# Kernel optimization log

Measured on AMD Instinct MI355X. Metric: run time of the kernel, lower is better.

## Reference

```python
import jax, jax.numpy as jnp
import numpy as np

TOP_K = 2
NUM_EXPERTS = 8


def setup_inputs() -> dict:
    key = jax.random.key(0)
    ks = jax.random.split(key, 9)
    B, S, N, H = 1, 8, 1024, 512
    E, I_moe, I_sh = NUM_EXPERTS, 2048 // TOP_K, 2048
    s = 0.02
    return {
        "hidden_states": jax.random.normal(ks[0], (B, S, N, H), dtype=jnp.float32),
        "gate_w": jax.random.normal(ks[1], (E, H), dtype=jnp.float32) * s,
        "expert_w1": jax.random.normal(ks[2], (E, I_moe, H), dtype=jnp.float32) * s,
        "expert_w2": jax.random.normal(ks[3], (E, H, I_moe), dtype=jnp.float32) * s,
        "expert_w3": jax.random.normal(ks[4], (E, I_moe, H), dtype=jnp.float32) * s,
        "shared_w1": jax.random.normal(ks[5], (I_sh, H), dtype=jnp.float32) * s,
        "shared_w2": jax.random.normal(ks[6], (H, I_sh), dtype=jnp.float32) * s,
        "shared_w3": jax.random.normal(ks[7], (I_sh, H), dtype=jnp.float32) * s,
        "shared_gate_w": jax.random.normal(ks[8], (1, H), dtype=jnp.float32) * s,
    }


def reference(hidden_states, gate_w, expert_w1, expert_w2, expert_w3,
              shared_w1, shared_w2, shared_w3, shared_gate_w):
    B, S, N, H = hidden_states.shape
    x = hidden_states.reshape(-1, H)                       # [T, H], T = B*S*N

    # Router: softmax in fp32, then top-k (norm_topk_prob=False).
    router_logits = x @ gate_w.T                           # [T, E]
    probs = jax.nn.softmax(router_logits.astype(jnp.float32), axis=-1)
    top_w, top_i = jax.lax.top_k(probs, TOP_K)             # [T, k]
    # Combine weight per (token, expert): zero for unselected experts.
    combine = jnp.sum(top_w[..., None] * jax.nn.one_hot(top_i, NUM_EXPERTS, dtype=probs.dtype), axis=1)
    combine = combine.astype(x.dtype)                      # [T, E]

    # Routed experts (SwiGLU FFN per expert), evaluated densely and masked
    # by the sparse combine weights (same math as gather/scatter dispatch).
    h1 = jnp.einsum('th,eih->tei', x, expert_w1)           # [T, E, I_moe]
    h3 = jnp.einsum('th,eih->tei', x, expert_w3)
    h = jax.nn.silu(h1) * h3
    expert_out = jnp.einsum('tei,ehi->teh', h, expert_w2)  # [T, E, H]
    moe_out = jnp.einsum('te,teh->th', combine, expert_out)

    # Shared expert with sigmoid gate.
    sh = (jax.nn.silu(x @ shared_w1.T) * (x @ shared_w3.T)) @ shared_w2.T
    sgate = jax.nn.sigmoid(x @ shared_gate_w.T)            # [T, 1]
    out = moe_out + sgate * sh

    return out.reshape(B, S, N, H), router_logits
```

## Files before the change

### kernel.cpp

```cpp
#include <hip/hip_runtime.h>
#include <hip/hip_bf16.h>
#include <stdint.h>
#include <math.h>

typedef __bf16 bf16;
typedef bf16 bf16x8 __attribute__((ext_vector_type(8)));
typedef bf16 bf16x4 __attribute__((ext_vector_type(4)));
typedef float f32x4 __attribute__((ext_vector_type(4)));
typedef unsigned int u32;

#define TOKENS 8192
#define HD 512
#define NE 8
#define IM 1024
#define ISH 2048
#define CAP 2560

__device__ __forceinline__ void gld16(const void* g, void* l) {
  __builtin_amdgcn_global_load_lds(
      (const __attribute__((address_space(1))) u32*)g,
      (__attribute__((address_space(3))) u32*)l, 16, 0, 0);
}

#define RT_BLOCKS (TOKENS / 4)
#define CVT_BLOCKS 3840
#define CVT_STRIDE (CVT_BLOCKS * 256)
#define F4_E  (NE * IM * HD / 4)
#define F4_S  (ISH * HD / 4)
#define F4_C1 (F4_E)
#define F4_C2 (F4_C1 + F4_E)
#define F4_C3 (F4_C2 + F4_S)
#define F4_C4 (F4_C3 + F4_S)
#define F4_C5 (F4_C4 + F4_E)
#define F4_TOT (F4_C5 + F4_S)

__launch_bounds__(256)
__global__ void router_cvt_k(const float* __restrict__ x, const float* __restrict__ gw,
                             const float* __restrict__ sgw, float* __restrict__ logits,
                             float* __restrict__ sgate, int* __restrict__ topi,
                             float* __restrict__ topw, int* __restrict__ counts,
                             bf16* __restrict__ xb,
                             const float* __restrict__ e1, const float* __restrict__ e3,
                             const float* __restrict__ s1, const float* __restrict__ s3,
                             const float* __restrict__ e2, const float* __restrict__ s2,
                             bf16* __restrict__ wdst) {
  if (blockIdx.x >= RT_BLOCKS) {
    int idx = (blockIdx.x - RT_BLOCKS) * 256 + threadIdx.x;
#pragma unroll
    for (int it = 0; it < 4; it++, idx += CVT_STRIDE) {
      const float* s; int off;
      if (idx < F4_C1)      { s = e1; off = idx; }
      else if (idx < F4_C2) { s = e3; off = idx - F4_C1; }
      else if (idx < F4_C3) { s = s1; off = idx - F4_C2; }
      else if (idx < F4_C4) { s = s3; off = idx - F4_C3; }
      else if (idx < F4_C5) { s = e2; off = idx - F4_C4; }
      else                  { s = s2; off = idx - F4_C5; }
      const float4 v = ((const float4*)s)[off];
      bf16x4 o;
      o.x = (bf16)v.x; o.y = (bf16)v.y; o.z = (bf16)v.z; o.w = (bf16)v.w;
      ((bf16x4*)wdst)[idx] = o;
    }
    return;
  }
  if (blockIdx.x == 0 && threadIdx.x < NE) counts[threadIdx.x] = 0;
  __shared__ float gws[9][512];
  for (int i = threadIdx.x; i < 9 * 512; i += 256) {
    int r = i >> 9, c = i & 511;
    float v = (r < 8) ? gw[i] : sgw[c];
    gws[r][((c & 7) << 6) | (c >> 3)] = v;
  }
  __syncthreads();
  int wave = threadIdx.x >> 6, lane = threadIdx.x & 63;
  int t = blockIdx.x * 4 + wave;
  const float* xp = x + (size_t)t * HD + lane * 8;
  float4 va = *(const float4*)xp;
  float4 vb = *(const float4*)(xp + 4);
  float xv[8] = {va.x, va.y, va.z, va.w, vb.x, vb.y, vb.z, vb.w};
  {
    bf16x8 xo;
#pragma unroll
    for (int j = 0; j < 8; j++) xo[j] = (bf16)xv[j];
    *(bf16x8*)(xb + (size_t)t * HD + lane * 8) = xo;
  }
  float acc[9];
#pragma unroll
  for (int e = 0; e < 9; e++) {
    float a = 0.f;
#pragma unroll
    for (int j = 0; j < 8; j++) a = fmaf(xv[j], gws[e][j * 64 + lane], a);
    acc[e] = a;
  }
#pragma unroll
  for (int off = 32; off > 0; off >>= 1) {
#pragma unroll
    for (int e = 0; e < 9; e++) acc[e] += __shfl_down(acc[e], off);
  }
  if (lane == 0) {
    float mx = acc[0];
#pragma unroll
    for (int e = 1; e < 8; e++) mx = fmaxf(mx, acc[e]);
    float p[8], sum = 0.f;
#pragma unroll
    for (int e = 0; e < 8; e++) { p[e] = expf(acc[e] - mx); sum += p[e]; }
    float inv = 1.f / sum;
    int i0 = 0; float b0 = p[0];
#pragma unroll
    for (int e = 1; e < 8; e++) if (p[e] > b0) { b0 = p[e]; i0 = e; }
    int i1 = -1; float b1 = -1.f;
#pragma unroll
    for (int e = 0; e < 8; e++) if (e != i0 && p[e] > b1) { b1 = p[e]; i1 = e; }
#pragma unroll
    for (int e = 0; e < 8; e++) logits[(size_t)t * 8 + e] = acc[e];
    topi[2 * t] = i0; topi[2 * t + 1] = i1;
    topw[2 * t] = b0 * inv; topw[2 * t + 1] = b1 * inv;
    sgate[t] = 1.f / (1.f + expf(-acc[8]));
  }
}

__launch_bounds__(256)
__global__ void dispatch_k(const int* __restrict__ topi, const float* __restrict__ topw,
                           int* __restrict__ counts, int* __restrict__ tok,
                           float* __restrict__ wl, int* __restrict__ pos) {
  __shared__ int lcnt[NE];
  __shared__ int lbase[NE];
  int tid = threadIdx.x;
  if (tid < NE) lcnt[tid] = 0;
  __syncthreads();
  int t = blockIdx.x * 256 + tid;
  int e0 = topi[2 * t], e1 = topi[2 * t + 1];
  float w0 = topw[2 * t], w1 = topw[2 * t + 1];
  int r0 = atomicAdd(&lcnt[e0], 1);
  int r1 = atomicAdd(&lcnt[e1], 1);
  __syncthreads();
  if (tid < NE) lbase[tid] = atomicAdd(&counts[tid], lcnt[tid]);
  __syncthreads();
  int p0 = lbase[e0] + r0;
  int p1 = lbase[e1] + r1;
  if (p0 < CAP) { tok[e0 * CAP + p0] = t; wl[e0 * CAP + p0] = w0; }
  if (p1 < CAP) { tok[e1 * CAP + p1] = t; wl[e1 * CAP + p1] = w1; }
  pos[2 * t]     = (p0 < CAP) ? e0 * CAP + p0 : -1;
  pos[2 * t + 1] = (p1 < CAP) ? e1 * CAP + p1 : -1;
}

__launch_bounds__(256, 4)
__global__ void gemm1_k(const bf16* __restrict__ X, const int* __restrict__ tokl,
                        const int* __restrict__ counts,
                        const bf16* __restrict__ e1w, const bf16* __restrict__ e3w,
                        const bf16* __restrict__ s1w, const bf16* __restrict__ s3w,
                        bf16* __restrict__ hmoe, bf16* __restrict__ hsh) {
  const bf16 *W1, *W3;
  bf16* Hout;
  const int* tl = nullptr;
  int cnt = 0, m0, n0, N;
  bool gather;
  int y = blockIdx.y;
  if (y < 160) {
    int e = y / 20, mt = y % 20;
    cnt = min(counts[e], CAP);
    if (mt * 128 >= cnt) return;
    gather = true;
    tl = tokl + e * CAP;
    W1 = e1w + (size_t)e * IM * HD;
    W3 = e3w + (size_t)e * IM * HD;
    Hout = hmoe + (size_t)e * CAP * IM;
    N = IM; m0 = mt * 128; n0 = blockIdx.x * 64;
  } else {
    int s = y - 160;
    gather = false;
    W1 = s1w; W3 = s3w; Hout = hsh; N = ISH;
    m0 = (s >> 1) * 128;
    n0 = ((s & 1) * 16 + blockIdx.x) * 64;
  }

  __shared__ __align__(16) bf16 As[2][128 * 32];
  __shared__ __align__(16) bf16 B1s[2][64 * 32];
  __shared__ __align__(16) bf16 B3s[2][64 * 32];

  int tid = threadIdx.x;
  int sr = tid >> 2;
  int colb = (tid & 3) * 16;
  int ar0, ar1;
  if (gather) {
    ar0 = tl[min(m0 + sr, cnt - 1)];
    ar1 = tl[min(m0 + 64 + sr, cnt - 1)];
  } else { ar0 = m0 + sr; ar1 = m0 + 64 + sr; }
  const char* apa = (const char*)(X + (size_t)ar0 * HD) + colb;
  const char* apb = (const char*)(X + (size_t)ar1 * HD) + colb;
  const char* bp1 = (const char*)(W1 + (size_t)(n0 + sr) * HD) + colb;
  const char* bp3 = (const char*)(W3 + (size_t)(n0 + sr) * HD) + colb;
  char* lA0a = (char*)&As[0][0] + tid * 16;
  char* lA0b = (char*)&As[1][0] + tid * 16;
  char* lA1a = (char*)&As[0][0] + 4096 + tid * 16;
  char* lA1b = (char*)&As[1][0] + 4096 + tid * 16;
  char* lB1a = (char*)&B1s[0][0] + tid * 16;
  char* lB1b = (char*)&B1s[1][0] + tid * 16;
  char* lB3a = (char*)&B3s[0][0] + tid * 16;
  char* lB3b = (char*)&B3s[1][0] + tid * 16;

  int wid = tid >> 6, lane = tid & 63;
  int wm = (wid >> 1) * 64, wn = (wid & 1) * 32;
  int lrow = lane & 15, lq = lane >> 4;

  f32x4 acc1[4][2] = {};
  f32x4 acc3[4][2] = {};

  for (int kb = 0; kb < 1024; kb += 128) {
    __syncthreads();
    gld16(apa + kb, lA0a);      gld16(apa + kb + 64, lA0b);
    gld16(apb + kb, lA1a);      gld16(apb + kb + 64, lA1b);
    gld16(bp1 + kb, lB1a);      gld16(bp1 + kb + 64, lB1b);
    gld16(bp3 + kb, lB3a);      gld16(bp3 + kb + 64, lB3b);
    __syncthreads();
#pragma unroll
    for (int ks = 0; ks < 2; ks++) {
      bf16x8 a[4], b1[2], b3[2];
#pragma unroll
      for (int i = 0; i < 4; i++)
        a[i] = *(const bf16x8*)&As[ks][(wm + i * 16 + lrow) * 32 + lq * 8];
#pragma unroll
      for (int j = 0; j < 2; j++) {
        b1[j] = *(const bf16x8*)&B1s[ks][(wn + j * 16 + lrow) * 32 + lq * 8];
        b3[j] = *(const bf16x8*)&B3s[ks][(wn + j * 16 + lrow) * 32 + lq * 8];
      }
#pragma unroll
      for (int i = 0; i < 4; i++)
#pragma unroll
        for (int j = 0; j < 2; j++) {
          acc1[i][j] = __builtin_amdgcn_mfma_f32_16x16x32_bf16(a[i], b1[j], acc1[i][j], 0, 0, 0);
          acc3[i][j] = __builtin_amdgcn_mfma_f32_16x16x32_bf16(a[i], b3[j], acc3[i][j], 0, 0, 0);
        }
    }
  }

#pragma unroll
  for (int i = 0; i < 4; i++)
#pragma unroll
    for (int r = 0; r < 4; r++) {
      int row = m0 + wm + i * 16 + lq * 4 + r;
#pragma unroll
      for (int j = 0; j < 2; j++) {
        float v1 = acc1[i][j][r], v3 = acc3[i][j][r];
        float hv = v1 / (1.f + __expf(-v1)) * v3;
        Hout[(size_t)row * N + (n0 + wn + j * 16 + lrow)] = (bf16)hv;
      }
    }
}

__launch_bounds__(256, 4)
__global__ void gemm2_k(const bf16* __restrict__ hmoe, const bf16* __restrict__ hsh,
                        const bf16* __restrict__ e2w, const bf16* __restrict__ s2w,
                        const float* __restrict__ wll, const int* __restrict__ counts,
                        bf16* __restrict__ yslot, bf16* __restrict__ ysh) {
  const bf16 *Hin, *W2;
  const float* wlp = nullptr;
  bf16* Yout;
  int cnt = 0, m0, K;
  bool weighted;
  int y = blockIdx.y;
  if (y < 64) {
    weighted = false;
    Hin = hsh; W2 = s2w; Yout = ysh; K = ISH; m0 = y * 128;
  } else {
    int e = (y - 64) / 20, mt = (y - 64) % 20;
    cnt = min(counts[e], CAP);
    if (mt * 128 >= cnt) return;
    weighted = true;
    Hin = hmoe + (size_t)e * CAP * IM;
    W2 = e2w + (size_t)e * HD * IM;
    wlp = wll + e * CAP;
    Yout = yslot + (size_t)e * CAP * HD;
    K = IM; m0 = mt * 128;
  }
  int n0 = blockIdx.x * 128;

  __shared__ __align__(16) bf16 As[2][128 * 32];
  __shared__ __align__(16) bf16 Bs[2][128 * 32];

  int tid = threadIdx.x;
  int sr = tid >> 2;
  int colb = (tid & 3) * 16;
  const char* apa = (const char*)(Hin + (size_t)(m0 + sr) * K) + colb;
  const char* apb = (const char*)(Hin + (size_t)(m0 + 64 + sr) * K) + colb;
  const char* bpa = (const char*)(W2 + (size_t)(n0 + sr) * K) + colb;
  const char* bpb = (const char*)(W2 + (size_t)(n0 + 64 + sr) * K) + colb;
  char* lA0a = (char*)&As[0][0] + tid * 16;
  char* lA0b = (char*)&As[1][0] + tid * 16;
  char* lA1a = (char*)&As[0][0] + 4096 + tid * 16;
  char* lA1b = (char*)&As[1][0] + 4096 + tid * 16;
  char* lB0a = (char*)&Bs[0][0] + tid * 16;
  char* lB0b = (char*)&Bs[1][0] + tid * 16;
  char* lB1a = (char*)&Bs[0][0] + 4096 + tid * 16;
  char* lB1b = (char*)&Bs[1][0] + 4096 + tid * 16;

  int wid = tid >> 6, lane = tid & 63;
  int wm = (wid >> 1) * 64, wn = (wid & 1) * 64;
  int lrow = lane & 15, lq = lane >> 4;

  f32x4 acc[4][4] = {};

  for (int kb = 0; kb < K * 2; kb += 128) {
    __syncthreads();
    gld16(apa + kb, lA0a);      gld16(apa + kb + 64, lA0b);
    gld16(apb + kb, lA1a);      gld16(apb + kb + 64, lA1b);
    gld16(bpa + kb, lB0a);      gld16(bpa + kb + 64, lB0b);
    gld16(bpb + kb, lB1a);      gld16(bpb + kb + 64, lB1b);
    __syncthreads();
#pragma unroll
    for (int ks = 0; ks < 2; ks++) {
      bf16x8 a[4], b[4];
#pragma unroll
      for (int i = 0; i < 4; i++) {
        a[i] = *(const bf16x8*)&As[ks][(wm + i * 16 + lrow) * 32 + lq * 8];
        b[i] = *(const bf16x8*)&Bs[ks][(wn + i * 16 + lrow) * 32 + lq * 8];
      }
#pragma unroll
      for (int i = 0; i < 4; i++)
#pragma unroll
        for (int j = 0; j < 4; j++)
          acc[i][j] = __builtin_amdgcn_mfma_f32_16x16x32_bf16(a[i], b[j], acc[i][j], 0, 0, 0);
    }
  }

#pragma unroll
  for (int i = 0; i < 4; i++)
#pragma unroll
    for (int r = 0; r < 4; r++) {
      int row = m0 + wm + i * 16 + lq * 4 + r;
      float w = weighted ? ((row < cnt) ? wlp[row] : 0.f) : 1.f;
      bf16* op = Yout + (size_t)row * HD;
#pragma unroll
      for (int j = 0; j < 4; j++)
        op[n0 + wn + j * 16 + lrow] = (bf16)(w * acc[i][j][r]);
    }
}

__launch_bounds__(256)
__global__ void combine_k(const bf16* __restrict__ yslot, const bf16* __restrict__ ysh,
                          const int* __restrict__ pos, const float* __restrict__ sgate,
                          float* __restrict__ out) {
  int wave = threadIdx.x >> 6, lane = threadIdx.x & 63;
  int t = blockIdx.x * 4 + wave;
  int p0 = pos[2 * t], p1 = pos[2 * t + 1];
  float g = sgate[t];
  int col = lane * 8;
  float acc[8];
  {
    const bf16x8 s = *(const bf16x8*)(ysh + (size_t)t * HD + col);
#pragma unroll
    for (int i = 0; i < 8; i++) acc[i] = g * (float)s[i];
  }
  if (p0 >= 0) {
    const bf16x8 v = *(const bf16x8*)(yslot + (size_t)p0 * HD + col);
#pragma unroll
    for (int i = 0; i < 8; i++) acc[i] += (float)v[i];
  }
  if (p1 >= 0) {
    const bf16x8 v = *(const bf16x8*)(yslot + (size_t)p1 * HD + col);
#pragma unroll
    for (int i = 0; i < 8; i++) acc[i] += (float)v[i];
  }
  float* op = out + (size_t)t * HD + col;
#pragma unroll
  for (int i = 0; i < 8; i++) op[i] = acc[i];
}

extern "C" void kernel_launch(void* const* d_in, const int* in_sizes, int n_in,
                              void* d_out, int out_size, void* d_ws, size_t ws_size,
                              hipStream_t stream) {
  const float* x   = (const float*)d_in[0];
  const float* gw  = (const float*)d_in[1];
  const float* ew1 = (const float*)d_in[2];
  const float* ew2 = (const float*)d_in[3];
  const float* ew3 = (const float*)d_in[4];
  const float* sw1 = (const float*)d_in[5];
  const float* sw2 = (const float*)d_in[6];
  const float* sw3 = (const float*)d_in[7];
  const float* sgw = (const float*)d_in[8];
  float* out = (float*)d_out;
  float* logits = out + (size_t)TOKENS * HD;

  char* w = (char*)d_ws;
  bf16* xb  = (bf16*)w; w += (size_t)TOKENS * HD * 2;
  bf16* e1b = (bf16*)w; w += (size_t)NE * IM * HD * 2;
  bf16* e3b = (bf16*)w; w += (size_t)NE * IM * HD * 2;
  bf16* s1b = (bf16*)w; w += (size_t)ISH * HD * 2;
  bf16* s3b = (bf16*)w; w += (size_t)ISH * HD * 2;
  bf16* e2b = (bf16*)w; w += (size_t)NE * HD * IM * 2;
  bf16* s2b = (bf16*)w; w += (size_t)HD * ISH * 2;
  float* sgate = (float*)w; w += TOKENS * 4;
  int*   topi  = (int*)w;   w += TOKENS * 2 * 4;
  float* topw  = (float*)w; w += TOKENS * 2 * 4;
  int*   counts = (int*)w;  w += 256;
  int*   tok   = (int*)w;   w += NE * CAP * 4;
  float* wl    = (float*)w; w += NE * CAP * 4;
  int*   pos   = (int*)w;   w += TOKENS * 2 * 4;
  bf16* hmoe = (bf16*)w; w += (size_t)NE * CAP * IM * 2;
  bf16* hsh  = (bf16*)w; w += (size_t)TOKENS * ISH * 2;
  bf16* yslot = xb;
  bf16* ysh   = (bf16*)((char*)xb + (size_t)NE * CAP * HD * 2);

  hipLaunchKernelGGL(router_cvt_k, dim3(RT_BLOCKS + CVT_BLOCKS), dim3(256), 0, stream,
                     x, gw, sgw, logits, sgate, topi, topw, counts, xb,
                     ew1, ew3, sw1, sw3, ew2, sw2, e1b);
  hipLaunchKernelGGL(dispatch_k, dim3(TOKENS / 256), dim3(256), 0, stream,
                     topi, topw, counts, tok, wl, pos);
  hipLaunchKernelGGL(gemm1_k, dim3(16, 160 + 128), dim3(256), 0, stream,
                     xb, tok, counts, e1b, e3b, s1b, s3b, hmoe, hsh);
  hipLaunchKernelGGL(gemm2_k, dim3(4, 64 + 160), dim3(256), 0, stream,
                     hmoe, hsh, e2b, s2b, wl, counts, yslot, ysh);
  hipLaunchKernelGGL(combine_k, dim3(TOKENS / 4), dim3(256), 0, stream,
                     yslot, ysh, pos, sgate, out);
}
```

Measured before the change: 264.0 us.

## Rewrite gate/up GEMM with 256x128 tiles, swizzled LDS and phased pipelining

```diff
diff --git a/kernel.cpp b/kernel.cpp
--- a/kernel.cpp
+++ b/kernel.cpp
@@ -142,7 +142,10 @@
   pos[2 * t + 1] = (p1 < CAP) ? e1 * CAP + p1 : -1;
 }
 
-__launch_bounds__(256, 4)
+#define LDSA(D) ((D) * 65536)
+#define LDSB(D) ((D) * 65536 + 32768)
+
+__launch_bounds__(512, 2)
 __global__ void gemm1_k(const bf16* __restrict__ X, const int* __restrict__ tokl,
                         const int* __restrict__ counts,
                         const bf16* __restrict__ e1w, const bf16* __restrict__ e3w,
@@ -154,96 +157,146 @@
   int cnt = 0, m0, n0, N;
   bool gather;
   int y = blockIdx.y;
-  if (y < 160) {
-    int e = y / 20, mt = y % 20;
+  if (y < 80) {
+    int e = y / 10, mt = y % 10;
     cnt = min(counts[e], CAP);
-    if (mt * 128 >= cnt) return;
+    if (mt * 256 >= cnt) return;
     gather = true;
     tl = tokl + e * CAP;
     W1 = e1w + (size_t)e * IM * HD;
     W3 = e3w + (size_t)e * IM * HD;
     Hout = hmoe + (size_t)e * CAP * IM;
-    N = IM; m0 = mt * 128; n0 = blockIdx.x * 64;
+    N = IM; m0 = mt * 256; n0 = blockIdx.x * 128;
   } else {
-    int s = y - 160;
+    int s = y - 80;
     gather = false;
     W1 = s1w; W3 = s3w; Hout = hsh; N = ISH;
-    m0 = (s >> 1) * 128;
-    n0 = ((s & 1) * 16 + blockIdx.x) * 64;
-  }
-
-  __shared__ __align__(16) bf16 As[2][128 * 32];
-  __shared__ __align__(16) bf16 B1s[2][64 * 32];
-  __shared__ __align__(16) bf16 B3s[2][64 * 32];
+    m0 = (s >> 1) * 256;
+    n0 = ((s & 1) * 8 + blockIdx.x) * 128;
+  }
+
+  __shared__ __align__(16) char smem[131072];
+  char* lds = (char*)smem;
 
   int tid = threadIdx.x;
-  int sr = tid >> 2;
-  int colb = (tid & 3) * 16;
-  int ar0, ar1;
+  int lane = tid & 63, wid = tid >> 6;
+  int wr = wid >> 2, wc = wid & 3;
+  int lrow = lane & 15, lq = lane >> 4;
+  int rs = (lq * 16) ^ ((lane & 4) << 3);
+  int aoff = wr * 16384 + lrow * 128 + rs;
+  int boff = 32768 + wc * 4096 + lrow * 128 + rs;
+  int rg = tid >> 3;
+  int colb = ((tid & 7) << 4) ^ (tid & 32);
+
+  const char *gA0, *gA1, *gA2, *gA3;
   if (gather) {
-    ar0 = tl[min(m0 + sr, cnt - 1)];
-    ar1 = tl[min(m0 + 64 + sr, cnt - 1)];
-  } else { ar0 = m0 + sr; ar1 = m0 + 64 + sr; }
-  const char* apa = (const char*)(X + (size_t)ar0 * HD) + colb;
-  const char* apb = (const char*)(X + (size_t)ar1 * HD) + colb;
-  const char* bp1 = (const char*)(W1 + (size_t)(n0 + sr) * HD) + colb;
-  const char* bp3 = (const char*)(W3 + (size_t)(n0 + sr) * HD) + colb;
-  char* lA0a = (char*)&As[0][0] + tid * 16;
-  char* lA0b = (char*)&As[1][0] + tid * 16;
-  char* lA1a = (char*)&As[0][0] + 4096 + tid * 16;
-  char* lA1b = (char*)&As[1][0] + 4096 + tid * 16;
-  char* lB1a = (char*)&B1s[0][0] + tid * 16;
-  char* lB1b = (char*)&B1s[1][0] + tid * 16;
-  char* lB3a = (char*)&B3s[0][0] + tid * 16;
-  char* lB3b = (char*)&B3s[1][0] + tid * 16;
-
-  int wid = tid >> 6, lane = tid & 63;
-  int wm = (wid >> 1) * 64, wn = (wid & 1) * 32;
-  int lrow = lane & 15, lq = lane >> 4;
-
-  f32x4 acc1[4][2] = {};
-  f32x4 acc3[4][2] = {};
-
-  for (int kb = 0; kb < 1024; kb += 128) {
-    __syncthreads();
-    gld16(apa + kb, lA0a);      gld16(apa + kb + 64, lA0b);
-    gld16(apb + kb, lA1a);      gld16(apb + kb + 64, lA1b);
-    gld16(bp1 + kb, lB1a);      gld16(bp1 + kb + 64, lB1b);
-    gld16(bp3 + kb, lB3a);      gld16(bp3 + kb + 64, lB3b);
-    __syncthreads();
-#pragma unroll
-    for (int ks = 0; ks < 2; ks++) {
-      bf16x8 a[4], b1[2], b3[2];
-#pragma unroll
-      for (int i = 0; i < 4; i++)
-        a[i] = *(const bf16x8*)&As[ks][(wm + i * 16 + lrow) * 32 + lq * 8];
-#pragma unroll
-      for (int j = 0; j < 2; j++) {
-        b1[j] = *(const bf16x8*)&B1s[ks][(wn + j * 16 + lrow) * 32 + lq * 8];
-        b3[j] = *(const bf16x8*)&B3s[ks][(wn + j * 16 + lrow) * 32 + lq * 8];
-      }
-#pragma unroll
-      for (int i = 0; i < 4; i++)
-#pragma unroll
-        for (int j = 0; j < 2; j++) {
-          acc1[i][j] = __builtin_amdgcn_mfma_f32_16x16x32_bf16(a[i], b1[j], acc1[i][j], 0, 0, 0);
-          acc3[i][j] = __builtin_amdgcn_mfma_f32_16x16x32_bf16(a[i], b3[j], acc3[i][j], 0, 0, 0);
-        }
-    }
-  }
-
-#pragma unroll
-  for (int i = 0; i < 4; i++)
+    gA0 = (const char*)(X + (size_t)tl[min(m0 + rg,       cnt - 1)] * HD) + colb;
+    gA1 = (const char*)(X + (size_t)tl[min(m0 + 64 + rg,  cnt - 1)] * HD) + colb;
+    gA2 = (const char*)(X + (size_t)tl[min(m0 + 128 + rg, cnt - 1)] * HD) + colb;
+    gA3 = (const char*)(X + (size_t)tl[min(m0 + 192 + rg, cnt - 1)] * HD) + colb;
+  } else {
+    gA0 = (const char*)(X + (size_t)(m0 + rg) * HD) + colb;
+    gA1 = (const char*)(X + (size_t)(m0 + 64 + rg) * HD) + colb;
+    gA2 = (const char*)(X + (size_t)(m0 + 128 + rg) * HD) + colb;
+    gA3 = (const char*)(X + (size_t)(m0 + 192 + rg) * HD) + colb;
+  }
+  const char* gBa = (const char*)(W1 + (size_t)(n0 + rg) * HD) + colb;
+  const char* gBb = (const char*)(W1 + (size_t)(n0 + 64 + rg) * HD) + colb;
+  const char* gBc = (const char*)(W3 + (size_t)(n0 + rg) * HD) + colb;
+  const char* gBd = (const char*)(W3 + (size_t)(n0 + 64 + rg) * HD) + colb;
+
+#define STG2(P0, O0, P1, O1, KT) { \
+    gld16(P0 + (KT) * 128, lds + (O0) + tid * 16); \
+    gld16(P1 + (KT) * 128, lds + (O1) + tid * 16); }
+#define STG_AQ0(D, KT) STG2(gA0, LDSA(D),         gA2, LDSA(D) + 16384, KT)
+#define STG_AQ1(D, KT) STG2(gA1, LDSA(D) + 8192,  gA3, LDSA(D) + 24576, KT)
+#define STG_B0(D, KT)  STG2(gBa, LDSB(D),         gBb, LDSB(D) + 8192,  KT)
+#define STG_B1(D, KT)  STG2(gBc, LDSB(D) + 16384, gBd, LDSB(D) + 24576, KT)
+
+  bf16x8 a[4][2], b1[2][2], b3[2][2];
+  f32x4 acc1[8][2] = {};
+  f32x4 acc3[8][2] = {};
+
+#define LD_A(D, IB) \
+  _Pragma("unroll") for (int i2 = 0; i2 < 4; i2++) \
+  _Pragma("unroll") for (int ks = 0; ks < 2; ks++) \
+    a[i2][ks] = *(const bf16x8*)(lds + (D) * 65536 + aoff + ((IB) + i2) * 2048 + ks * 64);
+#define LD_B(D, REG, EX) \
+  _Pragma("unroll") for (int j = 0; j < 2; j++) \
+  _Pragma("unroll") for (int ks = 0; ks < 2; ks++) \
+    REG[j][ks] = *(const bf16x8*)(lds + (D) * 65536 + boff + (EX) + j * 2048 + ks * 64);
+#define PH_MFMA(ACC, ILO, B) \
+  __builtin_amdgcn_s_barrier(); \
+  __builtin_amdgcn_s_setprio(1); \
+  _Pragma("unroll") for (int i2 = 0; i2 < 4; i2++) \
+  _Pragma("unroll") for (int j = 0; j < 2; j++) \
+  _Pragma("unroll") for (int ks = 0; ks < 2; ks++) \
+    ACC[(ILO) + i2][j] = __builtin_amdgcn_mfma_f32_16x16x32_bf16( \
+        a[i2][ks], B[j][ks], ACC[(ILO) + i2][j], 0, 0, 0); \
+  __builtin_amdgcn_s_setprio(0); \
+  __builtin_amdgcn_s_barrier();
+
+  STG_AQ0(0, 0); STG_B0(0, 0); STG_B1(0, 0); STG_AQ1(0, 0);
+  STG_AQ0(1, 1); STG_B1(1, 1); STG_AQ1(1, 1);
+  asm volatile("s_waitcnt vmcnt(6)" ::: "memory");
+  __builtin_amdgcn_s_barrier();
+
+#pragma unroll 1
+  for (int it = 0; it < 4; ++it) {
+    const int t2 = 2 * it + 2, t3 = 2 * it + 3;
+    const bool more = it < 3;
+    LD_A(0, 0); LD_B(0, b1, 0);
+    STG_B0(1, 2 * it + 1);
+    PH_MFMA(acc1, 0, b1)
+    LD_B(0, b3, 16384);
+    if (more) STG_AQ0(0, t2);
+    PH_MFMA(acc3, 0, b3)
+    LD_A(0, 4);
+    if (more) STG_B1(0, t2);
+    PH_MFMA(acc3, 4, b3)
+    if (more) STG_AQ1(0, t2);
+    if (more) { asm volatile("s_waitcnt vmcnt(6)" ::: "memory"); }
+    else      { asm volatile("s_waitcnt vmcnt(0)" ::: "memory"); }
+    PH_MFMA(acc1, 4, b1)
+    LD_A(1, 0); LD_B(1, b1, 0);
+    if (more) STG_B0(0, t2);
+    PH_MFMA(acc1, 0, b1)
+    LD_B(1, b3, 16384);
+    if (more) STG_AQ0(1, t3);
+    PH_MFMA(acc3, 0, b3)
+    LD_A(1, 4);
+    if (more) STG_B1(1, t3);
+    PH_MFMA(acc3, 4, b3)
+    if (more) STG_AQ1(1, t3);
+    if (more) { asm volatile("s_waitcnt vmcnt(6)" ::: "memory"); }
+    else      { asm volatile("s_waitcnt vmcnt(0)" ::: "memory"); }
+    PH_MFMA(acc1, 4, b1)
+  }
+
+  int orow0 = m0 + wr * 128;
+  int ocol0 = n0 + wc * 32 + lrow;
+#pragma unroll
+  for (int i = 0; i < 8; i++) {
 #pragma unroll
     for (int r = 0; r < 4; r++) {
-      int row = m0 + wm + i * 16 + lq * 4 + r;
+      int row = orow0 + i * 16 + lq * 4 + r;
+      bf16* op = Hout + (size_t)row * N + ocol0;
 #pragma unroll
       for (int j = 0; j < 2; j++) {
         float v1 = acc1[i][j][r], v3 = acc3[i][j][r];
         float hv = v1 / (1.f + __expf(-v1)) * v3;
-        Hout[(size_t)row * N + (n0 + wn + j * 16 + lrow)] = (bf16)hv;
+        op[j * 16] = (bf16)hv;
       }
     }
+  }
+#undef STG2
+#undef STG_AQ0
+#undef STG_AQ1
+#undef STG_B0
+#undef STG_B1
+#undef LD_A
+#undef LD_B
+#undef PH_MFMA
 }
 
 __launch_bounds__(256, 4)
@@ -404,7 +457,7 @@
                      ew1, ew3, sw1, sw3, ew2, sw2, e1b);
   hipLaunchKernelGGL(dispatch_k, dim3(TOKENS / 256), dim3(256), 0, stream,
                      topi, topw, counts, tok, wl, pos);
-  hipLaunchKernelGGL(gemm1_k, dim3(16, 160 + 128), dim3(256), 0, stream,
+  hipLaunchKernelGGL(gemm1_k, dim3(8, 80 + 64), dim3(512), 0, stream,
                      xb, tok, counts, e1b, e3b, s1b, s3b, hmoe, hsh);
   hipLaunchKernelGGL(gemm2_k, dim3(4, 64 + 160), dim3(256), 0, stream,
                      hmoe, hsh, e2b, s2b, wl, counts, yslot, ysh);
```

After: 296.2 us. 12.2% more time.
